# Performance work log

Hardware: AMD Instinct MI355X
Metric: run time of the kernel (lower is better)

The kernel has to match this reference:

```python
import jax, jax.numpy as jnp
import numpy as np

N, C, W_DIM, H_DIM = 2, 256, 64, 64
HEADS = 4
DH = C // HEADS  # per-head dim for Q,K,V projections
EPS = 1e-5


def _layernorm(x, w, b):
    mu = jnp.mean(x, axis=-1, keepdims=True)
    var = jnp.var(x, axis=-1, keepdims=True)
    return (x - mu) * jax.lax.rsqrt(var + EPS) * w + b


def setup_inputs() -> dict:
    key = jax.random.key(0)
    ks = jax.random.split(key, 12)
    s = 1.0 / np.sqrt(C)
    return {
        "x": jax.random.normal(ks[0], (N, C, W_DIM, H_DIM), dtype=jnp.float32),
        "ln1_w": jnp.ones((C,), jnp.float32),
        "ln1_b": jnp.zeros((C,), jnp.float32),
        # per-head projection weights, laid out for x @ W: [heads, C, DH]
        "WQ": jax.random.normal(ks[1], (HEADS, C, DH), jnp.float32) * s,
        "WK": jax.random.normal(ks[2], (HEADS, C, DH), jnp.float32) * s,
        "WV": jax.random.normal(ks[3], (HEADS, C, DH), jnp.float32) * s,
        "ln2_w": jnp.ones((C,), jnp.float32),
        "ln2_b": jnp.zeros((C,), jnp.float32),
        "W1": jax.random.normal(ks[4], (C, C), jnp.float32) * s,
        "b1": jnp.zeros((C,), jnp.float32),
        "W2": jax.random.normal(ks[5], (C, C), jnp.float32) * s,
        "b2": jnp.zeros((C,), jnp.float32),
    }


def reference(x, ln1_w, ln1_b, WQ, WK, WV, ln2_w, ln2_b, W1, b1, W2, b2):
    n, c, w, h = x.shape
    s = w * h
    # 'n c w h -> n (w h) c'
    r = x.reshape(n, c, s).transpose(0, 2, 1)          # [n, s, c]
    norm = _layernorm(r, ln1_w, ln1_b)
    # all heads at once (original loops over heads)
    Q = jnp.einsum('nsc,hcd->nhsd', norm, WQ)
    K = jnp.einsum('nsc,hcd->nhsd', norm, WK)
    V = jnp.einsum('nsc,hcd->nhsd', norm, WV)
    # scale is 1/sqrt(seq_len) per original (keys.shape[1])
    y = jnp.einsum('nhqd,nhkd->nhqk', Q, K) / jnp.sqrt(jnp.float32(s))
    # QUIRK: softmax over dim=1 of [n, q, k] => the QUERY axis (axis=2 here)
    z = jax.nn.softmax(y, axis=2)
    attn = jnp.einsum('nhqk,nhkd->nhqd', z, V)         # [n, h, s, dh]
    attn_cat = attn.transpose(0, 2, 1, 3).reshape(n, s, c)
    out = attn_cat + r
    out = _layernorm(out, ln2_w, ln2_b)
    out = jax.nn.gelu(out @ W1 + b1, approximate=False) @ W2 + b2
    out = out + attn_cat
    # 'n (w h) c -> n c w h'
    return out.transpose(0, 2, 1).reshape(n, c, w, h)
```

## Files before the change

### kernel.cpp

```cpp
#include <hip/hip_runtime.h>
#include <math.h>

#define SEQ 4096
#define CH  256
#define NHT 8
#define DHD 64

#define QSCALE 0.0225421092f

using bf16x8 = __attribute__((ext_vector_type(8))) short;
using f32x4  = __attribute__((ext_vector_type(4))) float;
typedef unsigned short u16;
typedef unsigned int   u32;

__device__ __forceinline__ u16 f2bf(float f) {
    u32 u = __float_as_uint(f);
    u = (u + 0x7fffu + ((u >> 16) & 1u)) >> 16;
    return (u16)u;
}
__device__ __forceinline__ float bf2f(u16 h) {
    return __uint_as_float(((u32)h) << 16);
}
__device__ __forceinline__ float fexp2(float x) {
    return __builtin_amdgcn_exp2f(x);
}

__global__ __launch_bounds__(256) void k_prep(const float* __restrict__ x,
                                              const float* __restrict__ ln1w,
                                              const float* __restrict__ ln1b,
                                              const float* __restrict__ WQ,
                                              const float* __restrict__ WK,
                                              const float* __restrict__ WV,
                                              const float* __restrict__ W1,
                                              const float* __restrict__ W2,
                                              u16* __restrict__ norm,
                                              u16* __restrict__ BtQKV,
                                              u16* __restrict__ W1t,
                                              u16* __restrict__ W2t)
{
    __shared__ float tile[32][257];
    __shared__ float mu[32], rs[32];
    int bid = blockIdx.x;
    int t = threadIdx.x;
    if (bid < 1280) {
        int id = bid * 256 + t;
        if (id < 768 * 256) {
            int j = id >> 8, c = id & 255;
            int which = j >> 8, h = (j >> 6) & 3, d = j & 63;
            const float* W = (which == 0) ? WQ : (which == 1) ? WK : WV;
            BtQKV[id] = f2bf(W[(h * 256 + c) * 64 + d]);
        } else if (id < 768 * 256 + 65536) {
            int jj = id - 768 * 256;
            int j = jj >> 8, c = jj & 255;
            W1t[jj] = f2bf(W1[c * 256 + j]);
        } else if (id < 768 * 256 + 2 * 65536) {
            int jj = id - 768 * 256 - 65536;
            int j = jj >> 8, c = jj & 255;
            W2t[jj] = f2bf(W2[c * 256 + j]);
        }
        return;
    }
    int b2i = bid - 1280;
    int n = b2i >> 7, s0 = (b2i & 127) * 32;
    int sl = t & 31, cg = t >> 5;
    for (int cc = 0; cc < 256; cc += 8) {
        int c = cc + cg;
        tile[sl][c] = x[(n * 256 + c) * SEQ + s0 + sl];
    }
    __syncthreads();
    int wv = t >> 6, l = t & 63;
    for (int rr = 0; rr < 8; rr++) {
        int s = wv * 8 + rr;
        float a0 = tile[s][l], a1 = tile[s][l + 64], a2 = tile[s][l + 128], a3 = tile[s][l + 192];
        float sm = a0 + a1 + a2 + a3;
        float sq = a0 * a0 + a1 * a1 + a2 * a2 + a3 * a3;
        for (int off = 32; off; off >>= 1) { sm += __shfl_xor(sm, off); sq += __shfl_xor(sq, off); }
        if (l == 0) {
            float m = sm * (1.f / 256.f);
            mu[s] = m;
            rs[s] = rsqrtf(sq * (1.f / 256.f) - m * m + 1e-5f);
        }
    }
    __syncthreads();
    float ww = ln1w[t], bb = ln1b[t];
    for (int s = 0; s < 32; s++) {
        float v = (tile[s][t] - mu[s]) * rs[s] * ww + bb;
        norm[(n * SEQ + s0 + s) * 256 + t] = f2bf(v);
    }
}

__global__ __launch_bounds__(256) void k_qkv(const u16* __restrict__ norm,
                                             const u16* __restrict__ Bt,
                                             u16* __restrict__ Qo,
                                             u16* __restrict__ Ko,
                                             float* __restrict__ Vfo)
{
    int m0 = blockIdx.x * 64, j0 = blockIdx.y * 128;
    int t = threadIdx.x, w = t >> 6, lane = t & 63, quad = lane >> 4, l16 = lane & 15;
    const u16* Ap = norm + (long)(m0 + w * 16 + l16) * 256;
    const u16* Bp = Bt + (long)j0 * 256;
    f32x4 z = {0.f, 0.f, 0.f, 0.f};
    f32x4 acc[8];
    #pragma unroll
    for (int j = 0; j < 8; j++) acc[j] = z;
    #pragma unroll
    for (int kc = 0; kc < 8; kc++) {
        bf16x8 a = *(const bf16x8*)&Ap[kc * 32 + quad * 8];
        #pragma unroll
        for (int j = 0; j < 8; j++) {
            bf16x8 b = *(const bf16x8*)&Bp[(long)(j * 16 + l16) * 256 + kc * 32 + quad * 8];
            acc[j] = __builtin_amdgcn_mfma_f32_16x16x32_bf16(a, b, acc[j], 0, 0, 0);
        }
    }
    #pragma unroll
    for (int j = 0; j < 8; j++) {
        int col = j0 + j * 16 + l16;
        int which = col >> 8, h = (col >> 6) & 3, d = col & 63;
        int m = m0 + w * 16 + quad * 4;
        int n = m >> 12, s = m & 4095;
        if (which == 2) {
            float4 o = make_float4(acc[j][0], acc[j][1], acc[j][2], acc[j][3]);
            *(float4*)&Vfo[((long)(n * 4 + h) * 64 + d) * SEQ + s] = o;
        } else {
            u16* dst = (which == 0) ? Qo : Ko;
            float sc = (which == 0) ? QSCALE : 1.0f;
            #pragma unroll
            for (int r = 0; r < 4; r++)
                dst[((n * 4 + h) * SEQ + s + r) * 64 + d] = f2bf(acc[j][r] * sc);
        }
    }
}

__device__ __forceinline__ void xcd_decode(int s, int& g, int& sub) {
    int xcd = s & 7, m = s >> 3;
    g = xcd * 2 + (m >> 5);
    sub = m & 31;
}
__device__ __forceinline__ void xcd_decode32(int s, int& g, int& sub) {
    int xcd = s & 7, m = s >> 3;
    g = xcd * 4 + (m >> 5);
    sub = m & 31;
}

__global__ __launch_bounds__(256, 3) void k_pass1(const u16* __restrict__ Q,
                                                  const u16* __restrict__ Km,
                                                  float* __restrict__ D2)
{
    __shared__ float Dred[128];
    int g, sub;
    xcd_decode32(blockIdx.x, g, sub);
    int nh = g & 7, qc = g >> 3, k0 = sub * 128;
    const u16* Qh = Q + (long)nh * SEQ * 64;
    const u16* Kh = Km + (long)nh * SEQ * 64;
    int t = threadIdx.x, w = t >> 6, lane = t & 63, quad = lane >> 4, l16 = lane & 15;
    bf16x8 Kf[8][2];
    #pragma unroll
    for (int i = 0; i < 8; i++) {
        Kf[i][0] = *(const bf16x8*)&Kh[(k0 + i * 16 + l16) * 64 + quad * 8];
        Kf[i][1] = *(const bf16x8*)&Kh[(k0 + i * 16 + l16) * 64 + 32 + quad * 8];
    }
    if (t < 128) Dred[t] = 0.f;
    f32x4 z = {0.f, 0.f, 0.f, 0.f};
    float Dacc[8][4] = {};
    const int qw0 = qc * 1024 + w * 256;

#define P1_LOADQ(B0, B1, ST)                                                  \
    {                                                                         \
        int _q = qw0 + (ST) * 16 + l16;                                       \
        B0 = *(const bf16x8*)&Qh[_q * 64 + quad * 8];                         \
        B1 = *(const bf16x8*)&Qh[_q * 64 + 32 + quad * 8];                    \
    }
#define P1_STEP(B0, B1)                                                       \
    {                                                                         \
        _Pragma("unroll")                                                     \
        for (int i = 0; i < 8; i++) {                                         \
            f32x4 acc = z;                                                    \
            acc = __builtin_amdgcn_mfma_f32_16x16x32_bf16(Kf[i][0], B0, acc, 0, 0, 0); \
            acc = __builtin_amdgcn_mfma_f32_16x16x32_bf16(Kf[i][1], B1, acc, 0, 0, 0); \
            _Pragma("unroll")                                                 \
            for (int r = 0; r < 4; r++) Dacc[i][r] += fexp2(acc[r]);          \
        }                                                                     \
    }

    bf16x8 qa0, qa1, qb0, qb1;
    P1_LOADQ(qa0, qa1, 0)
    P1_LOADQ(qb0, qb1, 1)
    for (int st = 0; st < 16; st += 2) {
        P1_STEP(qa0, qa1)
        if (st + 2 < 16) { P1_LOADQ(qa0, qa1, st + 2) }
        P1_STEP(qb0, qb1)
        if (st + 3 < 16) { P1_LOADQ(qb0, qb1, st + 3) }
    }
#undef P1_LOADQ
#undef P1_STEP

    #pragma unroll
    for (int i = 0; i < 8; i++)
        #pragma unroll
        for (int r = 0; r < 4; r++) {
            float v = Dacc[i][r];
            v += __shfl_xor(v, 1); v += __shfl_xor(v, 2);
            v += __shfl_xor(v, 4); v += __shfl_xor(v, 8);
            Dacc[i][r] = v;
        }
    __syncthreads();
    if (l16 == 0) {
        #pragma unroll
        for (int i = 0; i < 8; i++)
            #pragma unroll
            for (int r = 0; r < 4; r++)
                atomicAdd(&Dred[i * 16 + quad * 4 + r], Dacc[i][r]);
    }
    __syncthreads();
    if (t < 128) D2[((long)(qc * NHT + nh)) * SEQ + k0 + t] = Dred[t];
}

__global__ __launch_bounds__(256) void k_vdiv(const float* __restrict__ Vf,
                                              const float* __restrict__ D2,
                                              u16* __restrict__ Vto)
{
    int b = blockIdx.x;
    int nh = b >> 6, d = b & 63;
    const long QS = (long)NHT * SEQ;
    const float* Dp = D2 + (long)nh * SEQ;
    const float* src = Vf + ((long)nh * 64 + d) * SEQ;
    u16* dst = Vto + ((long)nh * 64 + d) * SEQ;
    int t = threadIdx.x;
    #pragma unroll
    for (int half = 0; half < 2; half++) {
        int k = half * 2048 + t * 8;
        float o[8];
        #pragma unroll
        for (int e = 0; e < 8; e++) {
            float dsum = Dp[k + e] + Dp[QS + k + e] + Dp[2 * QS + k + e] + Dp[3 * QS + k + e];
            o[e] = src[k + e] / dsum;
        }
        uint4 pk;
        pk.x = (u32)f2bf(o[0]) | ((u32)f2bf(o[1]) << 16);
        pk.y = (u32)f2bf(o[2]) | ((u32)f2bf(o[3]) << 16);
        pk.z = (u32)f2bf(o[4]) | ((u32)f2bf(o[5]) << 16);
        pk.w = (u32)f2bf(o[6]) | ((u32)f2bf(o[7]) << 16);
        *(uint4*)&dst[k] = pk;
    }
}

__global__ __launch_bounds__(256, 3) void k_pass2(const u16* __restrict__ Q,
                                                  const u16* __restrict__ Km,
                                                  const u16* __restrict__ Vt,
                                                  float* __restrict__ acat2)
{
    __shared__ __align__(16) u16 lP2[2][128][68];
    float (*red)[68] = (float(*)[68])lP2;

    int g, sub;
    xcd_decode(blockIdx.x, g, sub);
    int nh = g & 7, kcid = g >> 3, q0 = sub * 128;
    int n = nh >> 2, h = nh & 3;
    const u16* Qh = Q + (long)nh * SEQ * 64;
    const u16* Kh = Km + (long)nh * SEQ * 64;
    const u16* Vh = Vt + (long)nh * 64 * SEQ;
    int t = threadIdx.x, w = t >> 6, lane = t & 63, quad = lane >> 4, l16 = lane & 15;
    const int kblk = kcid * 2048;
    const int dw = w * 16 + l16;

    bf16x8 Qf[8][2];
    #pragma unroll
    for (int jq = 0; jq < 8; jq++)
        #pragma unroll
        for (int ch = 0; ch < 2; ch++)
            Qf[jq][ch] = *(const bf16x8*)&Qh[(q0 + jq * 16 + l16) * 64 + ch * 32 + quad * 8];

    f32x4 z = {0.f, 0.f, 0.f, 0.f};
    f32x4 acc[8];
    #pragma unroll
    for (int jq = 0; jq < 8; jq++) acc[jq] = z;

#define LOAD_K(KA, I)                                                         \
    {                                                                         \
        int _kb = kblk + (I) * 64 + w * 16;                                   \
        KA[0] = *(const bf16x8*)&Kh[(_kb + l16) * 64 + quad * 8];             \
        KA[1] = *(const bf16x8*)&Kh[(_kb + l16) * 64 + 32 + quad * 8];        \
    }
#define LOAD_V(VB, I)                                                         \
    {                                                                         \
        int _kb = kblk + (I) * 64;                                            \
        VB[0] = *(const bf16x8*)&Vh[(long)dw * SEQ + _kb + quad * 8];         \
        VB[1] = *(const bf16x8*)&Vh[(long)dw * SEQ + _kb + 32 + quad * 8];    \
    }
#define QK_STRIPE(KA, B)                                                      \
    {                                                                         \
        _Pragma("unroll")                                                     \
        for (int jq = 0; jq < 8; jq++) {                                      \
            f32x4 s_ = z;                                                     \
            s_ = __builtin_amdgcn_mfma_f32_16x16x32_bf16(KA[0], Qf[jq][0], s_, 0, 0, 0); \
            s_ = __builtin_amdgcn_mfma_f32_16x16x32_bf16(KA[1], Qf[jq][1], s_, 0, 0, 0); \
            u32 e0 = __float_as_uint(fexp2(s_[0]));                           \
            u32 e1 = __float_as_uint(fexp2(s_[1]));                           \
            u32 e2 = __float_as_uint(fexp2(s_[2]));                           \
            u32 e3 = __float_as_uint(fexp2(s_[3]));                           \
            uint2 pk;                                                         \
            pk.x = __builtin_amdgcn_perm(e1, e0, 0x07060302u);                \
            pk.y = __builtin_amdgcn_perm(e3, e2, 0x07060302u);                \
            *(uint2*)&lP2[B][jq * 16 + l16][w * 16 + quad * 4] = pk;          \
        }                                                                     \
    }
#define PV_STRIPE(VB, B)                                                      \
    {                                                                         \
        _Pragma("unroll")                                                     \
        for (int ks = 0; ks < 2; ks++) {                                      \
            _Pragma("unroll")                                                 \
            for (int jq = 0; jq < 8; jq++) {                                  \
                bf16x8 pa = *(const bf16x8*)&lP2[B][jq * 16 + l16][ks * 32 + quad * 8]; \
                acc[jq] = __builtin_amdgcn_mfma_f32_16x16x32_bf16(pa, VB[ks], acc[jq], 0, 0, 0); \
            }                                                                 \
        }                                                                     \
    }

    bf16x8 kA0[2], kA1[2], vb0[2], vb1[2];
    LOAD_K(kA0, 0)
    LOAD_V(vb0, 0)
    LOAD_K(kA1, 1)
    LOAD_V(vb1, 1)

    QK_STRIPE(kA0, 0)
    __syncthreads();
    for (int it = 0; it < 15; it++) {
        int i = it * 2;
        QK_STRIPE(kA1, 1)
        LOAD_K(kA0, i + 2)
        PV_STRIPE(vb0, 0)
        LOAD_V(vb0, i + 2)
        __syncthreads();
        QK_STRIPE(kA0, 0)
        LOAD_K(kA1, i + 3)
        PV_STRIPE(vb1, 1)
        LOAD_V(vb1, i + 3)
        __syncthreads();
    }
    QK_STRIPE(kA1, 1)
    PV_STRIPE(vb0, 0)
    __syncthreads();
    PV_STRIPE(vb1, 1)

#undef LOAD_K
#undef LOAD_V
#undef QK_STRIPE
#undef PV_STRIPE

    __syncthreads();
    #pragma unroll
    for (int jq = 0; jq < 8; jq++)
        #pragma unroll
        for (int r = 0; r < 4; r++)
            red[jq * 16 + quad * 4 + r][dw] = acc[jq][r];
    __syncthreads();
    float* dst = acat2 + (long)kcid * 8192 * 256;
    #pragma unroll
    for (int p = 0; p < 8; p++) {
        int row = p * 16 + (t >> 4);
        int ch = (t & 15) * 4;
        float4 o = *(float4*)&red[row][ch];
        *(float4*)&dst[((long)n * SEQ + q0 + row) * 256 + h * 64 + ch] = o;
    }
}

__global__ __launch_bounds__(256) void k_tail(const float* __restrict__ x,
                                              const float* __restrict__ acat2,
                                              const float* __restrict__ lnw,
                                              const float* __restrict__ lnb,
                                              const u16* __restrict__ W1t,
                                              const float* __restrict__ b1v,
                                              const u16* __restrict__ W2t,
                                              const float* __restrict__ b2v,
                                              float* __restrict__ out)
{
    __shared__ __align__(16) unsigned char smem[16448];
    float (*tile)[257] = (float(*)[257])smem;
    u16 (*lT)[264] = (u16(*)[264])smem;
    __shared__ float aF[16][257];
    __shared__ float mu[16], rs[16];
    __shared__ __align__(16) u16 lH[16][264];

    const long STRIDE = (long)8192 * 256;
    int m0 = blockIdx.x * 16;
    int n = m0 >> 12, s0 = m0 & 4095;
    int t = threadIdx.x, w = t >> 6, lane = t & 63, quad = lane >> 4, l16 = lane & 15;

    {
        int sl = t & 15, cg = t >> 4;
        for (int cc = 0; cc < 256; cc += 16) {
            int c = cc + cg;
            tile[sl][c] = x[(n * 256 + c) * SEQ + s0 + sl];
        }
    }
    __syncthreads();
    for (int s = 0; s < 16; s++) {
        long idx = (long)(m0 + s) * 256 + t;
        float a = acat2[idx] + acat2[idx + STRIDE];
        aF[s][t] = a;
        tile[s][t] += a;
    }
    __syncthreads();
    {
        int l = t & 63;
        for (int rr = 0; rr < 4; rr++) {
            int s = w * 4 + rr;
            float a0 = tile[s][l], a1 = tile[s][l + 64], a2 = tile[s][l + 128], a3 = tile[s][l + 192];
            float sm = a0 + a1 + a2 + a3;
            float sq = a0 * a0 + a1 * a1 + a2 * a2 + a3 * a3;
            for (int off = 32; off; off >>= 1) { sm += __shfl_xor(sm, off); sq += __shfl_xor(sq, off); }
            if (l == 0) {
                float m = sm * (1.f / 256.f);
                mu[s] = m;
                rs[s] = rsqrtf(sq * (1.f / 256.f) - m * m + 1e-5f);
            }
        }
    }
    __syncthreads();
    {
        float ww = lnw[t], bb = lnb[t];
        for (int s = 0; s < 16; s++)
            lH[s][t] = f2bf((tile[s][t] - mu[s]) * rs[s] * ww + bb);
    }
    __syncthreads();

    f32x4 z = {0.f, 0.f, 0.f, 0.f};
    f32x4 acc1[4];
    #pragma unroll
    for (int js = 0; js < 4; js++) acc1[js] = z;
    #pragma unroll
    for (int kc = 0; kc < 8; kc++) {
        bf16x8 b = *(const bf16x8*)&lH[l16][kc * 32 + quad * 8];
        #pragma unroll
        for (int js = 0; js < 4; js++) {
            bf16x8 a = *(const bf16x8*)&W1t[(long)(w * 64 + js * 16 + l16) * 256 + kc * 32 + quad * 8];
            acc1[js] = __builtin_amdgcn_mfma_f32_16x16x32_bf16(a, b, acc1[js], 0, 0, 0);
        }
    }
    #pragma unroll
    for (int js = 0; js < 4; js++) {
        u32 e[4];
        #pragma unroll
        for (int r = 0; r < 4; r++) {
            int j = w * 64 + js * 16 + quad * 4 + r;
            float v = acc1[js][r] + b1v[j];
            float g = 0.5f * v * (1.f + erff(v * 0.70710678118f));
            u32 u = __float_as_uint(g);
            e[r] = u + 0x7fffu + ((u >> 16) & 1u);
        }
        uint2 pk;
        pk.x = __builtin_amdgcn_perm(e[1], e[0], 0x07060302u);
        pk.y = __builtin_amdgcn_perm(e[3], e[2], 0x07060302u);
        *(uint2*)&lT[l16][w * 64 + js * 16 + quad * 4] = pk;
    }
    __syncthreads();
    f32x4 acc2[4];
    #pragma unroll
    for (int cs = 0; cs < 4; cs++) acc2[cs] = z;
    #pragma unroll
    for (int kc = 0; kc < 8; kc++) {
        bf16x8 pa = *(const bf16x8*)&lT[l16][kc * 32 + quad * 8];
        #pragma unroll
        for (int cs = 0; cs < 4; cs++) {
            bf16x8 wb = *(const bf16x8*)&W2t[(long)(w * 64 + cs * 16 + l16) * 256 + kc * 32 + quad * 8];
            acc2[cs] = __builtin_amdgcn_mfma_f32_16x16x32_bf16(pa, wb, acc2[cs], 0, 0, 0);
        }
    }
    #pragma unroll
    for (int cs = 0; cs < 4; cs++) {
        int c = w * 64 + cs * 16 + l16;
        float bj = b2v[c];
        float vv[4];
        #pragma unroll
        for (int r = 0; r < 4; r++)
            vv[r] = acc2[cs][r] + bj + aF[quad * 4 + r][c];
        float4 o = make_float4(vv[0], vv[1], vv[2], vv[3]);
        *(float4*)&out[((long)n * 256 + c) * SEQ + s0 + quad * 4] = o;
    }
}

extern "C" void kernel_launch(void* const* d_in, const int* in_sizes, int n_in,
                              void* d_out, int out_size, void* d_ws, size_t ws_size,
                              hipStream_t stream) {
    const float* x    = (const float*)d_in[0];
    const float* ln1w = (const float*)d_in[1];
    const float* ln1b = (const float*)d_in[2];
    const float* WQ   = (const float*)d_in[3];
    const float* WK   = (const float*)d_in[4];
    const float* WV   = (const float*)d_in[5];
    const float* ln2w = (const float*)d_in[6];
    const float* ln2b = (const float*)d_in[7];
    const float* W1   = (const float*)d_in[8];
    const float* b1   = (const float*)d_in[9];
    const float* W2   = (const float*)d_in[10];
    const float* b2   = (const float*)d_in[11];
    float* out = (float*)d_out;

    char* p = (char*)d_ws;
    u16* norm   = (u16*)p;   p += (size_t)8192 * 256 * 2;
    u16* BtQKV  = (u16*)p;   p += (size_t)768 * 256 * 2;
    u16* W1t    = (u16*)p;   p += (size_t)256 * 256 * 2;
    u16* W2t    = (u16*)p;   p += (size_t)256 * 256 * 2;
    u16* Qb     = (u16*)p;   p += (size_t)NHT * SEQ * 64 * 2;
    u16* Kb     = (u16*)p;   p += (size_t)NHT * SEQ * 64 * 2;
    u16* VtT    = (u16*)p;   p += (size_t)NHT * SEQ * 64 * 2;
    float* D2   = (float*)p; p += (size_t)4 * NHT * SEQ * 4;
    float* acat2= (float*)p; p += (size_t)2 * 8192 * 256 * 4;
    float* Vf   = acat2;

    k_prep<<<1536, 256, 0, stream>>>(x, ln1w, ln1b, WQ, WK, WV, W1, W2,
                                     norm, BtQKV, W1t, W2t);
    k_qkv<<<dim3(128, 6), 256, 0, stream>>>(norm, BtQKV, Qb, Kb, Vf);
    k_pass1<<<1024, 256, 0, stream>>>(Qb, Kb, D2);
    k_vdiv<<<512, 256, 0, stream>>>(Vf, D2, VtT);
    k_pass2<<<512, 256, 0, stream>>>(Qb, Kb, VtT, acat2);
    k_tail<<<512, 256, 0, stream>>>(x, acat2, ln2w, ln2b, W1t, b1, W2t, b2, out);
}
```

Measured before the change: 223.3 us.

## Reshape pass1 tiling to 64 keys by 2048 queries and vectorize vdiv

The column-softmax denominator pass now gives each block 64 keys and 2048 queries, so it needs only two query chunks instead of four. This halves the partial-sum buffer and the reads in the divide kernel, which now uses float4 loads. Fewer K fragments per thread lower register pressure, and launch bounds raise the occupancy target to 4 blocks. The trade-off is that each key tile is reused across fewer MFMAs per Q load, and the Q prefetch is now a simple one-step rotation.

```diff
diff --git a/kernel.cpp b/kernel.cpp
--- a/kernel.cpp
+++ b/kernel.cpp
@@ -136,66 +136,54 @@
     g = xcd * 2 + (m >> 5);
     sub = m & 31;
 }
-__device__ __forceinline__ void xcd_decode32(int s, int& g, int& sub) {
+__device__ __forceinline__ void xcd_decode64(int s, int& g, int& sub) {
     int xcd = s & 7, m = s >> 3;
-    g = xcd * 4 + (m >> 5);
-    sub = m & 31;
-}
-
-__global__ __launch_bounds__(256, 3) void k_pass1(const u16* __restrict__ Q,
+    g = xcd * 2 + (m >> 6);
+    sub = m & 63;
+}
+
+__global__ __launch_bounds__(256, 4) void k_pass1(const u16* __restrict__ Q,
                                                   const u16* __restrict__ Km,
                                                   float* __restrict__ D2)
 {
-    __shared__ float Dred[128];
+    __shared__ float Dred[64];
     int g, sub;
-    xcd_decode32(blockIdx.x, g, sub);
-    int nh = g & 7, qc = g >> 3, k0 = sub * 128;
+    xcd_decode64(blockIdx.x, g, sub);
+    int nh = g & 7, qc = g >> 3, k0 = sub * 64;
     const u16* Qh = Q + (long)nh * SEQ * 64;
     const u16* Kh = Km + (long)nh * SEQ * 64;
     int t = threadIdx.x, w = t >> 6, lane = t & 63, quad = lane >> 4, l16 = lane & 15;
-    bf16x8 Kf[8][2];
-    #pragma unroll
-    for (int i = 0; i < 8; i++) {
+    bf16x8 Kf[4][2];
+    #pragma unroll
+    for (int i = 0; i < 4; i++) {
         Kf[i][0] = *(const bf16x8*)&Kh[(k0 + i * 16 + l16) * 64 + quad * 8];
         Kf[i][1] = *(const bf16x8*)&Kh[(k0 + i * 16 + l16) * 64 + 32 + quad * 8];
     }
-    if (t < 128) Dred[t] = 0.f;
+    if (t < 64) Dred[t] = 0.f;
     f32x4 z = {0.f, 0.f, 0.f, 0.f};
-    float Dacc[8][4] = {};
-    const int qw0 = qc * 1024 + w * 256;
-
-#define P1_LOADQ(B0, B1, ST)                                                  \
-    {                                                                         \
-        int _q = qw0 + (ST) * 16 + l16;                                       \
-        B0 = *(const bf16x8*)&Qh[_q * 64 + quad * 8];                         \
-        B1 = *(const bf16x8*)&Qh[_q * 64 + 32 + quad * 8];                    \
-    }
-#define P1_STEP(B0, B1)                                                       \
-    {                                                                         \
-        _Pragma("unroll")                                                     \
-        for (int i = 0; i < 8; i++) {                                         \
-            f32x4 acc = z;                                                    \
-            acc = __builtin_amdgcn_mfma_f32_16x16x32_bf16(Kf[i][0], B0, acc, 0, 0, 0); \
-            acc = __builtin_amdgcn_mfma_f32_16x16x32_bf16(Kf[i][1], B1, acc, 0, 0, 0); \
-            _Pragma("unroll")                                                 \
-            for (int r = 0; r < 4; r++) Dacc[i][r] += fexp2(acc[r]);          \
-        }                                                                     \
-    }
-
-    bf16x8 qa0, qa1, qb0, qb1;
-    P1_LOADQ(qa0, qa1, 0)
-    P1_LOADQ(qb0, qb1, 1)
-    for (int st = 0; st < 16; st += 2) {
-        P1_STEP(qa0, qa1)
-        if (st + 2 < 16) { P1_LOADQ(qa0, qa1, st + 2) }
-        P1_STEP(qb0, qb1)
-        if (st + 3 < 16) { P1_LOADQ(qb0, qb1, st + 3) }
-    }
-#undef P1_LOADQ
-#undef P1_STEP
-
-    #pragma unroll
-    for (int i = 0; i < 8; i++)
+    float Dacc[4][4] = {};
+    const int qw0 = qc * 2048 + w * 512;
+    bf16x8 b0 = *(const bf16x8*)&Qh[(qw0 + l16) * 64 + quad * 8];
+    bf16x8 b1 = *(const bf16x8*)&Qh[(qw0 + l16) * 64 + 32 + quad * 8];
+    for (int step = 0; step < 32; step++) {
+        int q = qw0 + step * 16;
+        bf16x8 n0, n1;
+        if (step < 31) {
+            n0 = *(const bf16x8*)&Qh[(q + 16 + l16) * 64 + quad * 8];
+            n1 = *(const bf16x8*)&Qh[(q + 16 + l16) * 64 + 32 + quad * 8];
+        }
+        #pragma unroll
+        for (int i = 0; i < 4; i++) {
+            f32x4 acc = z;
+            acc = __builtin_amdgcn_mfma_f32_16x16x32_bf16(Kf[i][0], b0, acc, 0, 0, 0);
+            acc = __builtin_amdgcn_mfma_f32_16x16x32_bf16(Kf[i][1], b1, acc, 0, 0, 0);
+            #pragma unroll
+            for (int r = 0; r < 4; r++) Dacc[i][r] += fexp2(acc[r]);
+        }
+        b0 = n0; b1 = n1;
+    }
+    #pragma unroll
+    for (int i = 0; i < 4; i++)
         #pragma unroll
         for (int r = 0; r < 4; r++) {
             float v = Dacc[i][r];
@@ -206,13 +194,13 @@
     __syncthreads();
     if (l16 == 0) {
         #pragma unroll
-        for (int i = 0; i < 8; i++)
+        for (int i = 0; i < 4; i++)
             #pragma unroll
             for (int r = 0; r < 4; r++)
                 atomicAdd(&Dred[i * 16 + quad * 4 + r], Dacc[i][r]);
     }
     __syncthreads();
-    if (t < 128) D2[((long)(qc * NHT + nh)) * SEQ + k0 + t] = Dred[t];
+    if (t < 64) D2[((long)(qc * NHT + nh)) * SEQ + k0 + t] = Dred[t];
 }
 
 __global__ __launch_bounds__(256) void k_vdiv(const float* __restrict__ Vf,
@@ -221,20 +209,23 @@
 {
     int b = blockIdx.x;
     int nh = b >> 6, d = b & 63;
-    const long QS = (long)NHT * SEQ;
-    const float* Dp = D2 + (long)nh * SEQ;
+    const float* Da = D2 + (long)nh * SEQ;
+    const float* Db = Da + (long)NHT * SEQ;
     const float* src = Vf + ((long)nh * 64 + d) * SEQ;
     u16* dst = Vto + ((long)nh * 64 + d) * SEQ;
     int t = threadIdx.x;
     #pragma unroll
     for (int half = 0; half < 2; half++) {
         int k = half * 2048 + t * 8;
+        float4 va = *(const float4*)&src[k];
+        float4 vb = *(const float4*)&src[k + 4];
+        float4 a0 = *(const float4*)&Da[k], a1 = *(const float4*)&Da[k + 4];
+        float4 b0 = *(const float4*)&Db[k], b1 = *(const float4*)&Db[k + 4];
         float o[8];
-        #pragma unroll
-        for (int e = 0; e < 8; e++) {
-            float dsum = Dp[k + e] + Dp[QS + k + e] + Dp[2 * QS + k + e] + Dp[3 * QS + k + e];
-            o[e] = src[k + e] / dsum;
-        }
+        o[0] = va.x / (a0.x + b0.x); o[1] = va.y / (a0.y + b0.y);
+        o[2] = va.z / (a0.z + b0.z); o[3] = va.w / (a0.w + b0.w);
+        o[4] = vb.x / (a1.x + b1.x); o[5] = vb.y / (a1.y + b1.y);
+        o[6] = vb.z / (a1.z + b1.z); o[7] = vb.w / (a1.w + b1.w);
         uint4 pk;
         pk.x = (u32)f2bf(o[0]) | ((u32)f2bf(o[1]) << 16);
         pk.y = (u32)f2bf(o[2]) | ((u32)f2bf(o[3]) << 16);
@@ -504,7 +495,7 @@
     u16* Qb     = (u16*)p;   p += (size_t)NHT * SEQ * 64 * 2;
     u16* Kb     = (u16*)p;   p += (size_t)NHT * SEQ * 64 * 2;
     u16* VtT    = (u16*)p;   p += (size_t)NHT * SEQ * 64 * 2;
-    float* D2   = (float*)p; p += (size_t)4 * NHT * SEQ * 4;
+    float* D2   = (float*)p; p += (size_t)2 * NHT * SEQ * 4;
     float* acat2= (float*)p; p += (size_t)2 * 8192 * 256 * 4;
     float* Vf   = acat2;
 
```

Result: slower. 228.0 us (+2.1%).

## Split PV work across warps by d-half and k-half to reuse P fragments

Applied to the files above, without the earlier changes.

Changes the P·V work split so each warp owns a 32-wide slice of the head dimension and one half of each 64-key stripe. Previously each warp owned 16 d-columns over the full key range. Each P fragment read from shared memory now feeds two MFMAs, which halves LDS reads of P. The cost is double the accumulator registers (the occupancy hint drops from 3 to 2 waves) and an extra two-phase reduction across the k-halves in shared memory.

```diff
diff --git a/kernel.cpp b/kernel.cpp
--- a/kernel.cpp
+++ b/kernel.cpp
@@ -244,7 +244,7 @@
     }
 }
 
-__global__ __launch_bounds__(256, 3) void k_pass2(const u16* __restrict__ Q,
+__global__ __launch_bounds__(256, 2) void k_pass2(const u16* __restrict__ Q,
                                                   const u16* __restrict__ Km,
                                                   const u16* __restrict__ Vt,
                                                   float* __restrict__ acat2)
@@ -261,7 +261,7 @@
     const u16* Vh = Vt + (long)nh * 64 * SEQ;
     int t = threadIdx.x, w = t >> 6, lane = t & 63, quad = lane >> 4, l16 = lane & 15;
     const int kblk = kcid * 2048;
-    const int dw = w * 16 + l16;
+    const int dhalf = w >> 1, khalf = w & 1;
 
     bf16x8 Qf[8][2];
     #pragma unroll
@@ -271,9 +271,11 @@
             Qf[jq][ch] = *(const bf16x8*)&Qh[(q0 + jq * 16 + l16) * 64 + ch * 32 + quad * 8];
 
     f32x4 z = {0.f, 0.f, 0.f, 0.f};
-    f32x4 acc[8];
-    #pragma unroll
-    for (int jq = 0; jq < 8; jq++) acc[jq] = z;
+    f32x4 acc[8][2];
+    #pragma unroll
+    for (int jq = 0; jq < 8; jq++)
+        #pragma unroll
+        for (int jd = 0; jd < 2; jd++) acc[jq][jd] = z;
 
 #define LOAD_K(KA, I)                                                         \
     {                                                                         \
@@ -283,9 +285,9 @@
     }
 #define LOAD_V(VB, I)                                                         \
     {                                                                         \
-        int _kb = kblk + (I) * 64;                                            \
-        VB[0] = *(const bf16x8*)&Vh[(long)dw * SEQ + _kb + quad * 8];         \
-        VB[1] = *(const bf16x8*)&Vh[(long)dw * SEQ + _kb + 32 + quad * 8];    \
+        int _kb = kblk + (I) * 64 + khalf * 32;                               \
+        VB[0] = *(const bf16x8*)&Vh[(long)(dhalf * 32 + l16) * SEQ + _kb + quad * 8];      \
+        VB[1] = *(const bf16x8*)&Vh[(long)(dhalf * 32 + 16 + l16) * SEQ + _kb + quad * 8]; \
     }
 #define QK_STRIPE(KA, B)                                                      \
     {                                                                         \
@@ -307,12 +309,11 @@
 #define PV_STRIPE(VB, B)                                                      \
     {                                                                         \
         _Pragma("unroll")                                                     \
-        for (int ks = 0; ks < 2; ks++) {                                      \
+        for (int jq = 0; jq < 8; jq++) {                                      \
+            bf16x8 pa = *(const bf16x8*)&lP2[B][jq * 16 + l16][khalf * 32 + quad * 8]; \
             _Pragma("unroll")                                                 \
-            for (int jq = 0; jq < 8; jq++) {                                  \
-                bf16x8 pa = *(const bf16x8*)&lP2[B][jq * 16 + l16][ks * 32 + quad * 8]; \
-                acc[jq] = __builtin_amdgcn_mfma_f32_16x16x32_bf16(pa, VB[ks], acc[jq], 0, 0, 0); \
-            }                                                                 \
+            for (int jd = 0; jd < 2; jd++)                                    \
+                acc[jq][jd] = __builtin_amdgcn_mfma_f32_16x16x32_bf16(pa, VB[jd], acc[jq][jd], 0, 0, 0); \
         }                                                                     \
     }
 
@@ -348,11 +349,25 @@
 #undef PV_STRIPE
 
     __syncthreads();
-    #pragma unroll
-    for (int jq = 0; jq < 8; jq++)
-        #pragma unroll
-        for (int r = 0; r < 4; r++)
-            red[jq * 16 + quad * 4 + r][dw] = acc[jq][r];
+    if (khalf == 0) {
+        #pragma unroll
+        for (int jq = 0; jq < 8; jq++)
+            #pragma unroll
+            for (int jd = 0; jd < 2; jd++)
+                #pragma unroll
+                for (int r = 0; r < 4; r++)
+                    red[jq * 16 + quad * 4 + r][dhalf * 32 + jd * 16 + l16] = acc[jq][jd][r];
+    }
+    __syncthreads();
+    if (khalf == 1) {
+        #pragma unroll
+        for (int jq = 0; jq < 8; jq++)
+            #pragma unroll
+            for (int jd = 0; jd < 2; jd++)
+                #pragma unroll
+                for (int r = 0; r < 4; r++)
+                    red[jq * 16 + quad * 4 + r][dhalf * 32 + jd * 16 + l16] += acc[jq][jd][r];
+    }
     __syncthreads();
     float* dst = acat2 + (long)kcid * 8192 * 256;
     #pragma unroll
```

After: 218.1 us (median of 2 runs). -2.3%, faster.
